# Kernel tuning notes

Hardware: AMD Instinct MI355X
Metric: run time of the kernel (lower is better)

The kernel has to match this reference:

```python
import jax, jax.numpy as jnp
import numpy as np

P = 4  # patch_size


def setup_inputs() -> dict:
    key = jax.random.key(0)
    ks = jax.random.split(key, 5)
    B, H, W, C = 4, 256, 256, 256
    x = jax.random.normal(ks[0], (B, H, W, C), dtype=jnp.float32)
    scale = 1.0 / np.sqrt(C)
    Wq = jax.random.normal(ks[1], (C, C), dtype=jnp.float32) * scale
    bq = jax.random.normal(ks[2], (C,), dtype=jnp.float32) * 0.01
    Wo = jax.random.normal(ks[3], (C, C), dtype=jnp.float32) * scale
    bo = jax.random.normal(ks[4], (C,), dtype=jnp.float32) * 0.01
    return {"x": x, "Wq": Wq, "bq": bq, "Wo": Wo, "bo": bo}


def reference(x, Wq, bq, Wo, bo):
    p = P
    ps = p * p
    B, h, w, C = x.shape
    q_h, r_h = h // ps, (h % ps) // 2
    q_w, r_w = w // ps, (w % ps) // 2
    # centered crop to a multiple of p_square (identity when divisible)
    x = x[:, r_h:q_h * ps + r_h, r_w:q_w * ps + r_w, :]
    nH, nW = q_h * p, q_w * p  # number of p x p windows per axis
    # window partition: [B, nH, p, nW, p, C] -> [B, nH, nW, p*p, C]
    xw = x.reshape(B, nH, p, nW, p, C).transpose(0, 1, 3, 2, 4, 5)
    xw = xw.reshape(B, nH, nW, ps, C)
    # NOTE: source uses self.query for Q, K, and V (key/value layers unused)
    q = xw @ Wq.T + bq  # [B, nH, nW, p*p, C]
    scores = jnp.einsum('bhwic,bhwjc->bhwij', q, q)  # unscaled, per source
    attn = jax.nn.softmax(scores, axis=-1)
    z = jnp.einsum('bhwij,bhwjc->bhwic', attn, q)
    return z @ Wo.T + bo  # [B, nH, nW, p*p, C]
```

## Files before the change

kernel.cpp:

```cpp
#include <hip/hip_runtime.h>


typedef __attribute__((ext_vector_type(8))) short short8;
typedef __attribute__((ext_vector_type(4))) float floatx4;

static __device__ inline short f2bf(float f) {
    unsigned u = __float_as_uint(f);
    u = (u + 0x7FFFu + ((u >> 16) & 1u)) >> 16;
    return (short)u;
}
static __device__ inline short8 zero8() {
    short8 v;
#pragma unroll
    for (int k = 0; k < 8; ++k) v[k] = 0;
    return v;
}
static __device__ inline floatx4 zf4() {
    floatx4 v;
#pragma unroll
    for (int k = 0; k < 4; ++k) v[k] = 0.0f;
    return v;
}

__global__ void convert_weights(const float* __restrict__ Wq,
                                const float* __restrict__ Wo,
                                short* __restrict__ wbf) {
    int idx = blockIdx.x * 256 + threadIdx.x;
#pragma unroll
    for (int i = 0; i < 2; ++i) {
        int j = idx + i * 32768;
        wbf[j]         = f2bf(Wq[j]);
        wbf[65536 + j] = f2bf(Wo[j]);
    }
}

__global__ __launch_bounds__(256, 2) void lsa_fused(
    const float* __restrict__ x, const short* __restrict__ wbf,
    const float* __restrict__ bq, const float* __restrict__ bo,
    float* __restrict__ out) {
    __shared__ __align__(16) short Qrm[4][2][16 * 264];
    __shared__ __align__(16) short Pl[4][2][16 * 24];

    const int tid  = threadIdx.x;
    const int wv   = tid >> 6;
    const int lane = tid & 63;
    const int l15  = lane & 15;
    const int quad = lane >> 4;

    const int wid0 = (blockIdx.x * 4 + wv) * 2;
    const int pi = l15 >> 2, pj = l15 & 3;

    const float* xrow[2];
#pragma unroll
    for (int w = 0; w < 2; ++w) {
        int wid = wid0 + w;
        int b = wid >> 12, hp = (wid >> 6) & 63, wp = wid & 63;
        xrow[w] = x + ((size_t)b << 24) + ((size_t)((hp << 2) + pi) << 16)
                    + ((size_t)((wp << 2) + pj) << 8);
    }

    floatx4 acc[2][16];
#pragma unroll
    for (int w = 0; w < 2; ++w)
#pragma unroll
        for (int nt = 0; nt < 16; ++nt) acc[w][nt] = zf4();

    for (int kk = 0; kk < 8; ++kk) {
        short8 af[2];
#pragma unroll
        for (int w = 0; w < 2; ++w) {
            const float* p = xrow[w] + kk * 32 + quad * 8;
            float4 v0 = *(const float4*)p;
            float4 v1 = *(const float4*)(p + 4);
            short8 a;
            a[0] = f2bf(v0.x); a[1] = f2bf(v0.y); a[2] = f2bf(v0.z); a[3] = f2bf(v0.w);
            a[4] = f2bf(v1.x); a[5] = f2bf(v1.y); a[6] = f2bf(v1.z); a[7] = f2bf(v1.w);
            af[w] = a;
        }
#pragma unroll
        for (int nt = 0; nt < 16; ++nt) {
            short8 bfr = *(const short8*)(wbf + (nt * 16 + l15) * 256 + kk * 32 + quad * 8);
            acc[0][nt] = __builtin_amdgcn_mfma_f32_16x16x32_bf16(af[0], bfr, acc[0][nt], 0, 0, 0);
            acc[1][nt] = __builtin_amdgcn_mfma_f32_16x16x32_bf16(af[1], bfr, acc[1][nt], 0, 0, 0);
        }
    }

#pragma unroll
    for (int nt = 0; nt < 16; ++nt) {
        float bqv = bq[nt * 16 + l15];
#pragma unroll
        for (int w = 0; w < 2; ++w) {
            short* q = &Qrm[wv][w][0];
#pragma unroll
            for (int r = 0; r < 4; ++r)
                q[(quad * 4 + r) * 264 + nt * 16 + l15] = f2bf(acc[w][nt][r] + bqv);
        }
    }

#pragma unroll 1
    for (int w = 0; w < 2; ++w) {
        short* q  = &Qrm[wv][w][0];
        short* pl = &Pl[wv][w][0];

        floatx4 s = zf4();
#pragma unroll
        for (int kk = 0; kk < 8; ++kk) {
            short8 qf = *(const short8*)&q[l15 * 264 + kk * 32 + quad * 8];
            s = __builtin_amdgcn_mfma_f32_16x16x32_bf16(qf, qf, s, 0, 0, 0);
        }
        floatx4 p;
#pragma unroll
        for (int r = 0; r < 4; ++r) {
            float v = s[r];
            float m = v;
#pragma unroll
            for (int d = 1; d < 16; d <<= 1) m = fmaxf(m, __shfl_xor(m, d, 64));
            float e = __expf(v - m);
            float sum = e;
#pragma unroll
            for (int d = 1; d < 16; d <<= 1) sum += __shfl_xor(sum, d, 64);
            p[r] = e / sum;
        }
#pragma unroll
        for (int r = 0; r < 4; ++r)
            pl[(quad * 4 + r) * 24 + l15] = f2bf(p[r]);

        short8 pf = zero8();
        if (quad < 2) pf = *(const short8*)&pl[l15 * 24 + quad * 8];
        floatx4 z[16];
#pragma unroll
        for (int nt = 0; nt < 16; ++nt) {
            short8 qb = zero8();
            if (quad < 2) {
#pragma unroll
                for (int jj = 0; jj < 8; ++jj)
                    qb[jj] = q[(quad * 8 + jj) * 264 + nt * 16 + l15];
            }
            z[nt] = __builtin_amdgcn_mfma_f32_16x16x32_bf16(pf, qb, zf4(), 0, 0, 0);
        }
#pragma unroll
        for (int nt = 0; nt < 16; ++nt)
#pragma unroll
            for (int r = 0; r < 4; ++r)
                q[(quad * 4 + r) * 264 + nt * 16 + l15] = f2bf(z[nt][r]);
    }

#pragma unroll
    for (int w = 0; w < 2; ++w)
#pragma unroll
        for (int nt = 0; nt < 16; ++nt) acc[w][nt] = zf4();

    for (int kk = 0; kk < 8; ++kk) {
        short8 zf[2];
#pragma unroll
        for (int w = 0; w < 2; ++w)
            zf[w] = *(const short8*)&Qrm[wv][w][l15 * 264 + kk * 32 + quad * 8];
#pragma unroll
        for (int nt = 0; nt < 16; ++nt) {
            short8 bfr = *(const short8*)(wbf + 65536 + (nt * 16 + l15) * 256 + kk * 32 + quad * 8);
            acc[0][nt] = __builtin_amdgcn_mfma_f32_16x16x32_bf16(zf[0], bfr, acc[0][nt], 0, 0, 0);
            acc[1][nt] = __builtin_amdgcn_mfma_f32_16x16x32_bf16(zf[1], bfr, acc[1][nt], 0, 0, 0);
        }
    }

#pragma unroll
    for (int nt = 0; nt < 16; ++nt) {
        float bov = bo[nt * 16 + l15];
#pragma unroll
        for (int w = 0; w < 2; ++w) {
            float* orow = out + (size_t)(wid0 + w) * 4096;
#pragma unroll
            for (int r = 0; r < 4; ++r)
                orow[(quad * 4 + r) * 256 + nt * 16 + l15] = acc[w][nt][r] + bov;
        }
    }
}

extern "C" void kernel_launch(void* const* d_in, const int* in_sizes, int n_in,
                              void* d_out, int out_size, void* d_ws, size_t ws_size,
                              hipStream_t stream) {
    const float* x  = (const float*)d_in[0];
    const float* Wq = (const float*)d_in[1];
    const float* bq = (const float*)d_in[2];
    const float* Wo = (const float*)d_in[3];
    const float* bo = (const float*)d_in[4];
    float* out = (float*)d_out;
    short* wbf = (short*)d_ws;

    hipLaunchKernelGGL(convert_weights, dim3(128), dim3(256), 0, stream, Wq, Wo, wbf);
    hipLaunchKernelGGL(lsa_fused, dim3(2048), dim3(256), 0, stream,
                       x, wbf, bq, bo, out);
}
```

Baseline: 650.5 us.

## Keep Q in registers and reorder attention as P·(Z·WoT) without shared memory

Measured after the change: 645.3 us. No clear change (-0.8%).

```diff
diff --git a/kernel.cpp b/kernel.cpp
--- a/kernel.cpp
+++ b/kernel.cpp
@@ -2,18 +2,16 @@
 
 
 typedef __attribute__((ext_vector_type(8))) short short8;
+typedef __attribute__((ext_vector_type(4))) short short4v;
 typedef __attribute__((ext_vector_type(4))) float floatx4;
+
+#define MFMA32(a, b, c) __builtin_amdgcn_mfma_f32_16x16x32_bf16(a, b, c, 0, 0, 0)
+#define MFMA16(a, b, c) __builtin_amdgcn_mfma_f32_16x16x16bf16_1k(a, b, c, 0, 0, 0)
 
 static __device__ inline short f2bf(float f) {
     unsigned u = __float_as_uint(f);
     u = (u + 0x7FFFu + ((u >> 16) & 1u)) >> 16;
     return (short)u;
-}
-static __device__ inline short8 zero8() {
-    short8 v;
-#pragma unroll
-    for (int k = 0; k < 8; ++k) v[k] = 0;
-    return v;
 }
 static __device__ inline floatx4 zf4() {
     floatx4 v;
@@ -21,26 +19,39 @@
     for (int k = 0; k < 4; ++k) v[k] = 0.0f;
     return v;
 }
+static __device__ inline short8 cvt8(float4 v0, float4 v1) {
+    short8 a;
+    a[0] = f2bf(v0.x); a[1] = f2bf(v0.y); a[2] = f2bf(v0.z); a[3] = f2bf(v0.w);
+    a[4] = f2bf(v1.x); a[5] = f2bf(v1.y); a[6] = f2bf(v1.z); a[7] = f2bf(v1.w);
+    return a;
+}
+static __device__ inline short4v pack4(floatx4 a) {
+    short4v r;
+    r[0] = f2bf(a[0]); r[1] = f2bf(a[1]); r[2] = f2bf(a[2]); r[3] = f2bf(a[3]);
+    return r;
+}
+static __device__ inline short4v pack4b(floatx4 a, float4 b) {
+    short4v r;
+    r[0] = f2bf(a[0] + b.x); r[1] = f2bf(a[1] + b.y);
+    r[2] = f2bf(a[2] + b.z); r[3] = f2bf(a[3] + b.w);
+    return r;
+}
 
 __global__ void convert_weights(const float* __restrict__ Wq,
                                 const float* __restrict__ Wo,
                                 short* __restrict__ wbf) {
     int idx = blockIdx.x * 256 + threadIdx.x;
-#pragma unroll
-    for (int i = 0; i < 2; ++i) {
-        int j = idx + i * 32768;
-        wbf[j]         = f2bf(Wq[j]);
-        wbf[65536 + j] = f2bf(Wo[j]);
-    }
+    int n = idx >> 8, k = idx & 255;
+    wbf[idx] = f2bf(Wq[idx]);
+    int kk = k >> 4, q4 = (k >> 2) & 3, r = k & 3;
+    int pk = (kk >> 1) * 32 + q4 * 8 + (kk & 1) * 4 + r;
+    wbf[65536 + n * 256 + pk] = f2bf(Wo[idx]);
 }
 
-__global__ __launch_bounds__(256, 2) void lsa_fused(
+__global__ __launch_bounds__(256, 3) void lsa_fused(
     const float* __restrict__ x, const short* __restrict__ wbf,
     const float* __restrict__ bq, const float* __restrict__ bo,
     float* __restrict__ out) {
-    __shared__ __align__(16) short Qrm[4][2][16 * 264];
-    __shared__ __align__(16) short Pl[4][2][16 * 24];
-
     const int tid  = threadIdx.x;
     const int wv   = tid >> 6;
     const int lane = tid & 63;
@@ -59,119 +70,90 @@
                     + ((size_t)((wp << 2) + pj) << 8);
     }
 
-    floatx4 acc[2][16];
+    short8 xf[2][8];
 #pragma unroll
     for (int w = 0; w < 2; ++w)
 #pragma unroll
-        for (int nt = 0; nt < 16; ++nt) acc[w][nt] = zf4();
-
-    for (int kk = 0; kk < 8; ++kk) {
-        short8 af[2];
-#pragma unroll
-        for (int w = 0; w < 2; ++w) {
+        for (int kk = 0; kk < 8; ++kk) {
             const float* p = xrow[w] + kk * 32 + quad * 8;
             float4 v0 = *(const float4*)p;
             float4 v1 = *(const float4*)(p + 4);
-            short8 a;
-            a[0] = f2bf(v0.x); a[1] = f2bf(v0.y); a[2] = f2bf(v0.z); a[3] = f2bf(v0.w);
-            a[4] = f2bf(v1.x); a[5] = f2bf(v1.y); a[6] = f2bf(v1.z); a[7] = f2bf(v1.w);
-            af[w] = a;
+            xf[w][kk] = cvt8(v0, v1);
         }
+
+    short4v qf[2][16];
+#pragma unroll 2
+    for (int nt = 0; nt < 16; ++nt) {
+        floatx4 a0 = zf4(), a1 = zf4();
+        const short* wq = wbf + (nt * 16 + l15) * 256 + quad * 8;
 #pragma unroll
-        for (int nt = 0; nt < 16; ++nt) {
-            short8 bfr = *(const short8*)(wbf + (nt * 16 + l15) * 256 + kk * 32 + quad * 8);
-            acc[0][nt] = __builtin_amdgcn_mfma_f32_16x16x32_bf16(af[0], bfr, acc[0][nt], 0, 0, 0);
-            acc[1][nt] = __builtin_amdgcn_mfma_f32_16x16x32_bf16(af[1], bfr, acc[1][nt], 0, 0, 0);
+        for (int kk = 0; kk < 8; ++kk) {
+            short8 wf = *(const short8*)(wq + kk * 32);
+            a0 = MFMA32(wf, xf[0][kk], a0);
+            a1 = MFMA32(wf, xf[1][kk], a1);
         }
+        float4 b4 = *(const float4*)(bq + nt * 16 + quad * 4);
+        qf[0][nt] = pack4b(a0, b4);
+        qf[1][nt] = pack4b(a1, b4);
     }
 
+    floatx4 s0 = zf4(), s1 = zf4();
 #pragma unroll
     for (int nt = 0; nt < 16; ++nt) {
-        float bqv = bq[nt * 16 + l15];
-#pragma unroll
-        for (int w = 0; w < 2; ++w) {
-            short* q = &Qrm[wv][w][0];
-#pragma unroll
-            for (int r = 0; r < 4; ++r)
-                q[(quad * 4 + r) * 264 + nt * 16 + l15] = f2bf(acc[w][nt][r] + bqv);
-        }
+        s0 = MFMA16(qf[0][nt], qf[0][nt], s0);
+        s1 = MFMA16(qf[1][nt], qf[1][nt], s1);
     }
 
-#pragma unroll 1
+    short4v paf[2];
+#pragma unroll
     for (int w = 0; w < 2; ++w) {
-        short* q  = &Qrm[wv][w][0];
-        short* pl = &Pl[wv][w][0];
+        floatx4 s = w ? s1 : s0;
+        float m = fmaxf(fmaxf(s[0], s[1]), fmaxf(s[2], s[3]));
+        m = fmaxf(m, __shfl_xor(m, 16, 64));
+        m = fmaxf(m, __shfl_xor(m, 32, 64));
+        float e0 = __expf(s[0] - m), e1 = __expf(s[1] - m);
+        float e2 = __expf(s[2] - m), e3 = __expf(s[3] - m);
+        float sum = (e0 + e1) + (e2 + e3);
+        sum += __shfl_xor(sum, 16, 64);
+        sum += __shfl_xor(sum, 32, 64);
+        float inv = 1.0f / sum;
+        short4v pf;
+        pf[0] = f2bf(e0 * inv); pf[1] = f2bf(e1 * inv);
+        pf[2] = f2bf(e2 * inv); pf[3] = f2bf(e3 * inv);
+        paf[w] = pf;
+    }
 
-        floatx4 s = zf4();
+    short4v idf;
 #pragma unroll
-        for (int kk = 0; kk < 8; ++kk) {
-            short8 qf = *(const short8*)&q[l15 * 264 + kk * 32 + quad * 8];
-            s = __builtin_amdgcn_mfma_f32_16x16x32_bf16(qf, qf, s, 0, 0, 0);
+    for (int j = 0; j < 4; ++j) idf[j] = (l15 == quad * 4 + j) ? (short)0x3F80 : (short)0;
+
+    float* o0p = out + (size_t)wid0 * 4096;
+    float* o1p = o0p + 4096;
+
+#pragma unroll 2
+    for (int nt = 0; nt < 16; ++nt) {
+        floatx4 y0 = zf4(), y1 = zf4();
+        const short* wo = wbf + 65536 + (nt * 16 + l15) * 256 + quad * 8;
+#pragma unroll
+        for (int kk2 = 0; kk2 < 8; ++kk2) {
+            short8 wf = *(const short8*)(wo + kk2 * 32);
+            short4v wlo, whi;
+            wlo[0] = wf[0]; wlo[1] = wf[1]; wlo[2] = wf[2]; wlo[3] = wf[3];
+            whi[0] = wf[4]; whi[1] = wf[5]; whi[2] = wf[6]; whi[3] = wf[7];
+            y0 = MFMA16(wlo, qf[0][2 * kk2], y0);
+            y1 = MFMA16(wlo, qf[1][2 * kk2], y1);
+            y0 = MFMA16(whi, qf[0][2 * kk2 + 1], y0);
+            y1 = MFMA16(whi, qf[1][2 * kk2 + 1], y1);
         }
-        floatx4 p;
+        floatx4 t0 = MFMA16(pack4(y0), idf, zf4());
+        floatx4 t1 = MFMA16(pack4(y1), idf, zf4());
+        floatx4 o0 = MFMA16(paf[0], pack4(t0), zf4());
+        floatx4 o1 = MFMA16(paf[1], pack4(t1), zf4());
+        float bov = bo[nt * 16 + l15];
 #pragma unroll
         for (int r = 0; r < 4; ++r) {
-            float v = s[r];
-            float m = v;
-#pragma unroll
-            for (int d = 1; d < 16; d <<= 1) m = fmaxf(m, __shfl_xor(m, d, 64));
-            float e = __expf(v - m);
-            float sum = e;
-#pragma unroll
-            for (int d = 1; d < 16; d <<= 1) sum += __shfl_xor(sum, d, 64);
-            p[r] = e / sum;
-        }
-#pragma unroll
-        for (int r = 0; r < 4; ++r)
-            pl[(quad * 4 + r) * 24 + l15] = f2bf(p[r]);
-
-        short8 pf = zero8();
-        if (quad < 2) pf = *(const short8*)&pl[l15 * 24 + quad * 8];
-        floatx4 z[16];
-#pragma unroll
-        for (int nt = 0; nt < 16; ++nt) {
-            short8 qb = zero8();
-            if (quad < 2) {
-#pragma unroll
-                for (int jj = 0; jj < 8; ++jj)
-                    qb[jj] = q[(quad * 8 + jj) * 264 + nt * 16 + l15];
-            }
-            z[nt] = __builtin_amdgcn_mfma_f32_16x16x32_bf16(pf, qb, zf4(), 0, 0, 0);
-        }
-#pragma unroll
-        for (int nt = 0; nt < 16; ++nt)
-#pragma unroll
-            for (int r = 0; r < 4; ++r)
-                q[(quad * 4 + r) * 264 + nt * 16 + l15] = f2bf(z[nt][r]);
-    }
-
-#pragma unroll
-    for (int w = 0; w < 2; ++w)
-#pragma unroll
-        for (int nt = 0; nt < 16; ++nt) acc[w][nt] = zf4();
-
-    for (int kk = 0; kk < 8; ++kk) {
-        short8 zf[2];
-#pragma unroll
-        for (int w = 0; w < 2; ++w)
-            zf[w] = *(const short8*)&Qrm[wv][w][l15 * 264 + kk * 32 + quad * 8];
-#pragma unroll
-        for (int nt = 0; nt < 16; ++nt) {
-            short8 bfr = *(const short8*)(wbf + 65536 + (nt * 16 + l15) * 256 + kk * 32 + quad * 8);
-            acc[0][nt] = __builtin_amdgcn_mfma_f32_16x16x32_bf16(zf[0], bfr, acc[0][nt], 0, 0, 0);
-            acc[1][nt] = __builtin_amdgcn_mfma_f32_16x16x32_bf16(zf[1], bfr, acc[1][nt], 0, 0, 0);
-        }
-    }
-
-#pragma unroll
-    for (int nt = 0; nt < 16; ++nt) {
-        float bov = bo[nt * 16 + l15];
-#pragma unroll
-        for (int w = 0; w < 2; ++w) {
-            float* orow = out + (size_t)(wid0 + w) * 4096;
-#pragma unroll
-            for (int r = 0; r < 4; ++r)
-                orow[(quad * 4 + r) * 256 + nt * 16 + l15] = acc[w][nt][r] + bov;
+            o0p[(quad * 4 + r) * 256 + nt * 16 + l15] = o0[r] + bov;
+            o1p[(quad * 4 + r) * 256 + nt * 16 + l15] = o1[r] + bov;
         }
     }
 }
@@ -187,7 +169,7 @@
     float* out = (float*)d_out;
     short* wbf = (short*)d_ws;
 
-    hipLaunchKernelGGL(convert_weights, dim3(128), dim3(256), 0, stream, Wq, Wo, wbf);
+    hipLaunchKernelGGL(convert_weights, dim3(256), dim3(256), 0, stream, Wq, Wo, wbf);
     hipLaunchKernelGGL(lsa_fused, dim3(2048), dim3(256), 0, stream,
                        x, wbf, bq, bo, out);
 }
```
